# Performance work log

Measured on AMD Instinct MI355X. Metric: run time of the kernel, lower is better.

## Reference

```python
import jax, jax.numpy as jnp
import numpy as np

CROP_H = 14
CROP_W = 14
EXTRAPOLATION_VALUE = 0.0


def setup_inputs() -> dict:
    key = jax.random.key(0)
    k1, k2, k3 = jax.random.split(key, 3)
    image = jax.random.normal(k1, (8, 256, 100, 152), dtype=jnp.float32)
    # normalized box coords in [0,1]; (y1,x1,y2,x2), y2<y1 allowed (extrapolation handles it)
    boxes = jax.random.uniform(k2, (1000, 4), dtype=jnp.float32)
    box_ind = jax.random.randint(k3, (1000,), 0, 8, dtype=jnp.int32)
    return {"image": image, "boxes": boxes, "box_ind": box_ind}


def _crop_and_resize(image, boxes, box_ind):
    # image: [B, C, H, W]; boxes: [N, 4] (y1, x1, y2, x2) normalized; box_ind: [N]
    B, C, H, W = image.shape
    dt = image.dtype
    y1, x1, y2, x2 = boxes[:, 0], boxes[:, 1], boxes[:, 2], boxes[:, 3]

    # TF crop_and_resize sampling grid (crop size > 1 path)
    h_scale = (y2 - y1) * (H - 1) / (CROP_H - 1)          # [N]
    w_scale = (x2 - x1) * (W - 1) / (CROP_W - 1)          # [N]
    in_y = y1[:, None] * (H - 1) + jnp.arange(CROP_H, dtype=dt)[None, :] * h_scale[:, None]  # [N, ch]
    in_x = x1[:, None] * (W - 1) + jnp.arange(CROP_W, dtype=dt)[None, :] * w_scale[:, None]  # [N, cw]

    valid_y = (in_y >= 0) & (in_y <= H - 1)               # [N, ch]
    valid_x = (in_x >= 0) & (in_x <= W - 1)               # [N, cw]

    top = jnp.floor(in_y)
    left = jnp.floor(in_x)
    y_lerp = in_y - top                                    # [N, ch]
    x_lerp = in_x - left                                   # [N, cw]

    ti = jnp.clip(top, 0, H - 1).astype(jnp.int32)         # top index    [N, ch]
    bi = jnp.clip(top + 1, 0, H - 1).astype(jnp.int32)     # bottom index [N, ch]
    li = jnp.clip(left, 0, W - 1).astype(jnp.int32)        # left index   [N, cw]
    ri = jnp.clip(left + 1, 0, W - 1).astype(jnp.int32)    # right index  [N, cw]

    b = box_ind[:, None, None]                             # [N, 1, 1]
    yt = ti[:, :, None]
    yb = bi[:, :, None]
    xl = li[:, None, :]
    xr = ri[:, None, :]

    # mixed advanced indexing -> gathered dims first: [N, ch, cw, C]
    tl = image[b, :, yt, xl]
    tr = image[b, :, yt, xr]
    bl = image[b, :, yb, xl]
    br = image[b, :, yb, xr]

    xw = x_lerp[:, None, :, None]                          # [N, 1, cw, 1]
    yw = y_lerp[:, :, None, None]                          # [N, ch, 1, 1]
    top_v = tl + (tr - tl) * xw
    bot_v = bl + (br - bl) * xw
    val = top_v + (bot_v - top_v) * yw                     # [N, ch, cw, C]

    valid = (valid_y[:, :, None] & valid_x[:, None, :])[..., None]
    out = jnp.where(valid, val, jnp.asarray(EXTRAPOLATION_VALUE, dt))
    return jnp.transpose(out, (0, 3, 1, 2))                # [N, C, ch, cw]


def reference(image, boxes, box_ind):
    return _crop_and_resize(image, boxes, box_ind)
```

## Files before the change

kernel.cpp:

```cpp
#include <hip/hip_runtime.h>

#define CROP_H 14
#define CROP_W 14
#define IMG_B 8
#define IMG_C 256
#define IMG_H 100
#define IMG_W 152
#define NBOX 1000
#define PLANE (IMG_H * IMG_W)
#define POS (CROP_H * CROP_W)
#define PAIRS (POS / 2)
#define OUT_PER_BOX (IMG_C * POS)
#define BOXCAP 64
#define CG 32
#define NCG (IMG_C / CG)

typedef float f2u __attribute__((ext_vector_type(2), aligned(8)));
typedef float f4u __attribute__((ext_vector_type(4), aligned(16)));

__global__ __launch_bounds__(1024) void sort_boxes_kernel(
    const int* __restrict__ box_ind,
    int* __restrict__ perm,
    int* __restrict__ offsets)
{
    __shared__ unsigned s_mask[IMG_B][32];
    __shared__ int s_tot[IMG_B];
    const int tid = threadIdx.x;

    if (tid < IMG_B * 32) ((unsigned*)s_mask)[tid] = 0u;
    __syncthreads();

    int key = 0;
    if (tid < NBOX) {
        key = box_ind[tid];
        atomicOr(&s_mask[key][tid >> 5], 1u << (tid & 31));
    }
    __syncthreads();

    if (tid < IMG_B) {
        int t = 0;
        #pragma unroll
        for (int w = 0; w < 32; ++w) t += __popc(s_mask[tid][w]);
        s_tot[tid] = t;
    }
    __syncthreads();

    if (tid == 0) {
        int acc = 0;
        #pragma unroll
        for (int k = 0; k < IMG_B; ++k) { offsets[k] = acc; acc += s_tot[k]; }
        offsets[IMG_B] = acc;
    }

    if (tid < NBOX) {
        int base = 0;
        #pragma unroll
        for (int k = 0; k < IMG_B; ++k) base += (k < key) ? s_tot[k] : 0;
        const int w = tid >> 5, b = tid & 31;
        int r = __popc(s_mask[key][w] & ((b == 0) ? 0u : ((1u << b) - 1u)));
        for (int ww = 0; ww < w; ++ww) r += __popc(s_mask[key][ww]);
        perm[base + r] = tid;
    }
}

__global__ __launch_bounds__(1024, 8) void CropAndResize_16630113370849_kernel(
    const float* __restrict__ image,
    const float* __restrict__ boxes,
    const int* __restrict__ perm,
    const int* __restrict__ offsets,
    float* __restrict__ out)
{
    __shared__ __align__(16) float s_plane[PLANE];
    __shared__ f2u s_row[BOXCAP * CROP_H];
    __shared__ f4u s_colp[BOXCAP * 7];
    __shared__ unsigned s_ob[BOXCAP];

    const int c   = blockIdx.x;
    const int b   = blockIdx.y;
    const int tid = threadIdx.x;

    {
        const float4* __restrict__ src =
            (const float4*)(image + ((size_t)b * IMG_C + c) * PLANE);
        float4* dst = (float4*)s_plane;
        #pragma unroll
        for (int i = 0; i < 4; ++i) {
            const int e = i * 1024 + tid;
            if (e < PLANE / 4) dst[e] = src[e];
        }
    }

    const int s0 = offsets[b], s1 = offsets[b + 1];
    const unsigned cPOS = (unsigned)(c * POS);

    for (int ck = s0; ck < s1; ck += BOXCAP) {
        const int cnt = min(BOXCAP, s1 - ck);

        __syncthreads();

        for (int j = tid; j < cnt * 21; j += 1024) {
            const int slot = j / 21;
            const int t    = j - slot * 21;
            const int n    = perm[ck + slot];
            if (t == 0) s_ob[slot] = (unsigned)(n * OUT_PER_BOX);

            const float y1 = boxes[n * 4 + 0];
            const float x1 = boxes[n * 4 + 1];
            const float y2 = boxes[n * 4 + 2];
            const float x2 = boxes[n * 4 + 3];

            if (t < CROP_H) {
                const float hs   = __fdiv_rn(__fmul_rn(__fsub_rn(y2, y1), (float)(IMG_H - 1)),
                                             (float)(CROP_H - 1));
                const float in_y = __fadd_rn(__fmul_rn(y1, (float)(IMG_H - 1)),
                                             __fmul_rn((float)t, hs));
                const int vy = (in_y >= 0.0f) && (in_y <= (float)(IMG_H - 1));
                const float top = floorf(in_y);
                const float yw  = __fsub_rn(in_y, top);
                const int ti = (int)fminf(fmaxf(top, 0.0f), (float)(IMG_H - 1));
                const int r0 = min(ti, IMG_H - 2);
                const int sely = (ti == IMG_H - 1);
                f2u e; e.x = __int_as_float((r0 * IMG_W) | (sely << 14) | (vy << 15));
                e.y = yw;
                s_row[slot * CROP_H + t] = e;
            } else {
                const int xg = t - CROP_H;
                const float ws = __fdiv_rn(__fmul_rn(__fsub_rn(x2, x1), (float)(IMG_W - 1)),
                                           (float)(CROP_W - 1));
                const float x1W = __fmul_rn(x1, (float)(IMG_W - 1));
                f4u e;
                #pragma unroll
                for (int k = 0; k < 2; ++k) {
                    const int x = 2 * xg + k;
                    const float in_x = __fadd_rn(x1W, __fmul_rn((float)x, ws));
                    const int vx = (in_x >= 0.0f) && (in_x <= (float)(IMG_W - 1));
                    const float left = floorf(in_x);
                    const float xw   = __fsub_rn(in_x, left);
                    const int li = (int)fminf(fmaxf(left, 0.0f), (float)(IMG_W - 1));
                    const int c0 = min(li, IMG_W - 2);
                    const int selx = (li == IMG_W - 1);
                    const int bits = c0 | (selx << 8) | (vx << 9);
                    if (k == 0) { e.x = __int_as_float(bits); e.y = xw; }
                    else        { e.z = __int_as_float(bits); e.w = xw; }
                }
                s_colp[slot * 7 + xg] = e;
            }
        }
        __syncthreads();

        const int total = cnt * PAIRS;
        for (int q = tid; q < total; q += 1024) {
            const int slot = q / PAIRS;
            const int rem  = q - slot * PAIRS;
            const int y    = rem / 7;
            const int xg   = rem - y * 7;

            const f2u re = s_row[slot * CROP_H + y];
            const f4u ce = s_colp[slot * 7 + xg];
            const int ri  = __float_as_int(re.x);
            const float yw = re.y;
            const int offr = ri & 0x3FFF;
            const bool sely = (ri & 0x4000) != 0;
            const bool vy   = (ri & 0x8000) != 0;

            f2u res;
            #pragma unroll
            for (int k = 0; k < 2; ++k) {
                const int ci   = __float_as_int(k ? ce.z : ce.x);
                const float xw = k ? ce.w : ce.y;
                const float* pp = s_plane + (offr + (ci & 0xFF));
                const float a0 = pp[0];
                const float a1 = pp[1];
                const float b0 = pp[IMG_W];
                const float b1 = pp[IMG_W + 1];

                const float tA = sely ? b0 : a0;
                const float tB = sely ? b1 : a1;
                const float tl = (ci & 0x100) ? tB : tA;
                const float bl = (ci & 0x100) ? b1 : b0;

                const float top_v = __fadd_rn(tl, __fmul_rn(__fsub_rn(tB, tl), xw));
                const float bot_v = __fadd_rn(bl, __fmul_rn(__fsub_rn(b1, bl), xw));
                const float v = __fadd_rn(top_v, __fmul_rn(__fsub_rn(bot_v, top_v), yw));
                const bool vald = vy && (ci & 0x200);
                res[k] = vald ? v : 0.0f;
            }

            *(f2u*)(out + (size_t)(s_ob[slot] + cPOS + (unsigned)(2 * q - slot * POS + 0)
                                   - (unsigned)(2 * rem) + (unsigned)(y * CROP_W + 2 * xg))) = res;
        }
    }
}

__global__ __launch_bounds__(256) void crop_chw_kernel(
    const float* __restrict__ image,
    const float* __restrict__ boxes,
    const int* __restrict__ box_ind,
    float* __restrict__ out)
{
    const int bid  = blockIdx.x;
    const int cg   = bid & 7;
    const int n    = bid >> 3;
    const int tid  = threadIdx.x;
    if (tid >= POS) return;

    const int b = box_ind[n];
    const int y = tid / CROP_W;
    const int x = tid - y * CROP_W;

    const float y1 = boxes[n * 4 + 0];
    const float x1 = boxes[n * 4 + 1];
    const float y2 = boxes[n * 4 + 2];
    const float x2 = boxes[n * 4 + 3];

    const float hs   = __fdiv_rn(__fmul_rn(__fsub_rn(y2, y1), (float)(IMG_H - 1)),
                                 (float)(CROP_H - 1));
    const float in_y = __fadd_rn(__fmul_rn(y1, (float)(IMG_H - 1)),
                                 __fmul_rn((float)y, hs));
    const int vy = (in_y >= 0.0f) && (in_y <= (float)(IMG_H - 1));
    const float top = floorf(in_y);
    const float yw  = __fsub_rn(in_y, top);
    const int ti = (int)fminf(fmaxf(top, 0.0f), (float)(IMG_H - 1));

    const float ws   = __fdiv_rn(__fmul_rn(__fsub_rn(x2, x1), (float)(IMG_W - 1)),
                                 (float)(CROP_W - 1));
    const float in_x = __fadd_rn(__fmul_rn(x1, (float)(IMG_W - 1)),
                                 __fmul_rn((float)x, ws));
    const int vx = (in_x >= 0.0f) && (in_x <= (float)(IMG_W - 1));
    const float left = floorf(in_x);
    const float xw   = __fsub_rn(in_x, left);
    const int li = (int)fminf(fmaxf(left, 0.0f), (float)(IMG_W - 1));

    const int r0 = min(ti, IMG_H - 2);
    const int c0 = min(li, IMG_W - 2);
    const bool sely = (ti == IMG_H - 1);
    const bool selx = (li == IMG_W - 1);
    const bool vald = (vy & vx) != 0;

    const float* __restrict__ pl =
        image + (size_t)b * (size_t)(IMG_C * PLANE)
              + (size_t)(cg * CG) * PLANE + (r0 * IMG_W + c0);
    float* __restrict__ po =
        out + (size_t)n * (size_t)OUT_PER_BOX + (size_t)(cg * CG) * POS + tid;

    #pragma unroll 8
    for (int cl = 0; cl < CG; ++cl) {
        const float2 ra = *(const float2*)(pl);
        const float2 rb = *(const float2*)(pl + IMG_W);
        const float tA = sely ? rb.x : ra.x;
        const float tB = sely ? rb.y : ra.y;
        const float tl = selx ? tB : tA;
        const float bl = selx ? rb.y : rb.x;
        const float top_v = __fadd_rn(tl, __fmul_rn(__fsub_rn(tB, tl), xw));
        const float bot_v = __fadd_rn(bl, __fmul_rn(__fsub_rn(rb.y, bl), xw));
        const float v = __fadd_rn(top_v, __fmul_rn(__fsub_rn(bot_v, top_v), yw));
        *po = vald ? v : 0.0f;
        pl += PLANE;
        po += POS;
    }
}

extern "C" void kernel_launch(void* const* d_in, const int* in_sizes, int n_in,
                              void* d_out, int out_size, void* d_ws, size_t ws_size,
                              hipStream_t stream) {
    const float* image  = (const float*)d_in[0];
    const float* boxes  = (const float*)d_in[1];
    const int*   boxind = (const int*)d_in[2];
    float* out = (float*)d_out;

    const size_t need = (NBOX + IMG_B + 1) * sizeof(int);
    if (ws_size >= need) {
        int* perm    = (int*)d_ws;
        int* offsets = perm + NBOX;

        sort_boxes_kernel<<<1, 1024, 0, stream>>>(boxind, perm, offsets);
        CropAndResize_16630113370849_kernel<<<dim3(IMG_C, IMG_B), 1024, 0, stream>>>(
            image, boxes, perm, offsets, out);
    } else {
        crop_chw_kernel<<<dim3(NBOX * NCG), 256, 0, stream>>>(
            image, boxes, boxind, out);
    }
}
```

Baseline: 100.1 us.

## Process two channels per block to amortize per-box coordinate setup

```diff
diff --git a/kernel.cpp b/kernel.cpp
--- a/kernel.cpp
+++ b/kernel.cpp
@@ -12,6 +12,7 @@
 #define PAIRS (POS / 2)
 #define OUT_PER_BOX (IMG_C * POS)
 #define BOXCAP 64
+#define NCP (IMG_C / 2)
 #define CG 32
 #define NCG (IMG_C / CG)
 
@@ -63,35 +64,35 @@
     }
 }
 
-__global__ __launch_bounds__(1024, 8) void CropAndResize_16630113370849_kernel(
+__global__ __launch_bounds__(1024, 4) void CropAndResize_16630113370849_kernel(
     const float* __restrict__ image,
     const float* __restrict__ boxes,
     const int* __restrict__ perm,
     const int* __restrict__ offsets,
     float* __restrict__ out)
 {
-    __shared__ __align__(16) float s_plane[PLANE];
+    __shared__ __align__(16) float s_plane[2 * PLANE];
     __shared__ f2u s_row[BOXCAP * CROP_H];
     __shared__ f4u s_colp[BOXCAP * 7];
     __shared__ unsigned s_ob[BOXCAP];
 
-    const int c   = blockIdx.x;
+    const int cp  = blockIdx.x;
     const int b   = blockIdx.y;
     const int tid = threadIdx.x;
 
     {
         const float4* __restrict__ src =
-            (const float4*)(image + ((size_t)b * IMG_C + c) * PLANE);
+            (const float4*)(image + ((size_t)b * IMG_C + 2 * cp) * PLANE);
         float4* dst = (float4*)s_plane;
         #pragma unroll
-        for (int i = 0; i < 4; ++i) {
+        for (int i = 0; i < 8; ++i) {
             const int e = i * 1024 + tid;
-            if (e < PLANE / 4) dst[e] = src[e];
+            if (e < (2 * PLANE) / 4) dst[e] = src[e];
         }
     }
 
     const int s0 = offsets[b], s1 = offsets[b + 1];
-    const unsigned cPOS = (unsigned)(c * POS);
+    const unsigned cbase = (unsigned)(2 * cp * POS);
 
     for (int ck = s0; ck < s1; ck += BOXCAP) {
         const int cnt = min(BOXCAP, s1 - ck);
@@ -149,6 +150,7 @@
         __syncthreads();
 
         const int total = cnt * PAIRS;
+        #pragma unroll 2
         for (int q = tid; q < total; q += 1024) {
             const int slot = q / PAIRS;
             const int rem  = q - slot * PAIRS;
@@ -157,37 +159,53 @@
 
             const f2u re = s_row[slot * CROP_H + y];
             const f4u ce = s_colp[slot * 7 + xg];
-            const int ri  = __float_as_int(re.x);
+            const int   ri = __float_as_int(re.x);
             const float yw = re.y;
-            const int offr = ri & 0x3FFF;
+            const int  offr = ri & 0x3FFF;
             const bool sely = (ri & 0x4000) != 0;
             const bool vy   = (ri & 0x8000) != 0;
 
-            f2u res;
+            const int   ci0 = __float_as_int(ce.x);
+            const float xw0 = ce.y;
+            const int   ci1 = __float_as_int(ce.z);
+            const float xw1 = ce.w;
+            const int  base0 = offr + (ci0 & 0xFF);
+            const int  base1 = offr + (ci1 & 0xFF);
+            const bool sx0 = (ci0 & 0x100) != 0, v0 = vy && (ci0 & 0x200);
+            const bool sx1 = (ci1 & 0x100) != 0, v1 = vy && (ci1 & 0x200);
+
+            const unsigned outoff = s_ob[slot] + cbase + (unsigned)(y * CROP_W + 2 * xg);
+
             #pragma unroll
-            for (int k = 0; k < 2; ++k) {
-                const int ci   = __float_as_int(k ? ce.z : ce.x);
-                const float xw = k ? ce.w : ce.y;
-                const float* pp = s_plane + (offr + (ci & 0xFF));
-                const float a0 = pp[0];
-                const float a1 = pp[1];
-                const float b0 = pp[IMG_W];
-                const float b1 = pp[IMG_W + 1];
-
-                const float tA = sely ? b0 : a0;
-                const float tB = sely ? b1 : a1;
-                const float tl = (ci & 0x100) ? tB : tA;
-                const float bl = (ci & 0x100) ? b1 : b0;
-
-                const float top_v = __fadd_rn(tl, __fmul_rn(__fsub_rn(tB, tl), xw));
-                const float bot_v = __fadd_rn(bl, __fmul_rn(__fsub_rn(b1, bl), xw));
-                const float v = __fadd_rn(top_v, __fmul_rn(__fsub_rn(bot_v, top_v), yw));
-                const bool vald = vy && (ci & 0x200);
-                res[k] = vald ? v : 0.0f;
+            for (int pc = 0; pc < 2; ++pc) {
+                const float* __restrict__ P = s_plane + pc * PLANE;
+                f2u res;
+                {
+                    const float a0 = P[base0], a1 = P[base0 + 1];
+                    const float b0 = P[base0 + IMG_W], b1 = P[base0 + IMG_W + 1];
+                    const float tA = sely ? b0 : a0;
+                    const float tB = sely ? b1 : a1;
+                    const float tl = sx0 ? tB : tA;
+                    const float bl = sx0 ? b1 : b0;
+                    const float top_v = __fadd_rn(tl, __fmul_rn(__fsub_rn(tB, tl), xw0));
+                    const float bot_v = __fadd_rn(bl, __fmul_rn(__fsub_rn(b1, bl), xw0));
+                    const float v = __fadd_rn(top_v, __fmul_rn(__fsub_rn(bot_v, top_v), yw));
+                    res.x = v0 ? v : 0.0f;
+                }
+                {
+                    const float a0 = P[base1], a1 = P[base1 + 1];
+                    const float b0 = P[base1 + IMG_W], b1 = P[base1 + IMG_W + 1];
+                    const float tA = sely ? b0 : a0;
+                    const float tB = sely ? b1 : a1;
+                    const float tl = sx1 ? tB : tA;
+                    const float bl = sx1 ? b1 : b0;
+                    const float top_v = __fadd_rn(tl, __fmul_rn(__fsub_rn(tB, tl), xw1));
+                    const float bot_v = __fadd_rn(bl, __fmul_rn(__fsub_rn(b1, bl), xw1));
+                    const float v = __fadd_rn(top_v, __fmul_rn(__fsub_rn(bot_v, top_v), yw));
+                    res.y = v1 ? v : 0.0f;
+                }
+                *(f2u*)(out + (size_t)(outoff + (unsigned)(pc * POS))) = res;
             }
-
-            *(f2u*)(out + (size_t)(s_ob[slot] + cPOS + (unsigned)(2 * q - slot * POS + 0)
-                                   - (unsigned)(2 * rem) + (unsigned)(y * CROP_W + 2 * xg))) = res;
         }
     }
 }
@@ -274,7 +292,7 @@
         int* offsets = perm + NBOX;
 
         sort_boxes_kernel<<<1, 1024, 0, stream>>>(boxind, perm, offsets);
-        CropAndResize_16630113370849_kernel<<<dim3(IMG_C, IMG_B), 1024, 0, stream>>>(
+        CropAndResize_16630113370849_kernel<<<dim3(NCP, IMG_B), 1024, 0, stream>>>(
             image, boxes, perm, offsets, out);
     } else {
         crop_chw_kernel<<<dim3(NBOX * NCG), 256, 0, stream>>>(
```

New measurement: 102.3 us. 2.3% more time.
